# Kernel tuning notes

Measured on AMD Instinct MI355X. Metric: run time of the kernel, lower is better.

The kernel has to match this reference:

```python
import jax, jax.numpy as jnp
import numpy as np
from jax import lax

SIGMA = 0.8
THRESH_MIN = 50.0
THRESH_MAX = 80.0
TRACK_CONN = 5
TRACK_ITERS = 3


def _gaussian_kernel(sigma=SIGMA):
    ks = int(((sigma - 0.8) / 0.3 + 1) * 2 + 1)
    ks += 1 if ks % 2 == 0 else 0
    ax = np.arange(-ks // 2 + 1.0, ks // 2 + 1.0)
    xx, yy = np.meshgrid(ax, ax)
    normal = 1 / (2.0 * np.pi * sigma ** 2)
    k = np.exp(-(xx ** 2 + yy ** 2) / (2.0 * sigma ** 2)) * normal
    k = k / np.sum(k)
    return k.reshape(ks, ks, 1, 1).astype(np.float32)


def _sobel_kernel():
    gx = np.array([[-1, 0, 1], [-2, 0, 2], [-1, 0, 1]], dtype=np.float32)
    gy = np.array([[1, 2, 1], [0, 0, 0], [-1, -2, -1]], dtype=np.float32)
    return np.stack([gx, gy], axis=-1).reshape(3, 3, 1, 2)


def setup_inputs() -> dict:
    key = jax.random.key(0)
    x = jax.random.uniform(key, (8, 1024, 1024, 1), dtype=jnp.float32) * 255.0
    return {
        'x': x,
        'gaussian_kernel': jnp.asarray(_gaussian_kernel()),
        'sobel_kernel': jnp.asarray(_sobel_kernel()),
    }


def _conv_same(x, k):
    return lax.conv_general_dilated(x, k, (1, 1), 'SAME',
                                    dimension_numbers=('NHWC', 'HWIO', 'NHWC'))


# offsets with kernel value 0 (others are -inf) for the 4 angle NMS kernels
_ANGLE_OFFSETS = [
    [(0, -1), (0, 0), (0, 1)],     # 0 deg
    [(-1, 1), (0, 0), (1, -1)],    # 45 deg
    [(-1, 0), (0, 0), (1, 0)],     # 90 deg
    [(-1, -1), (0, 0), (1, 1)],    # 135 deg
]


def _angle_dilation(ar):
    # morphological dilation (tf.nn.dilation2d) with -inf masked 3x3 kernels,
    # realized as max over the 3 unmasked shifts per angle channel.
    B, H, W, _ = ar.shape
    pad = jnp.pad(ar, ((0, 0), (1, 1), (1, 1), (0, 0)),
                  constant_values=-jnp.inf)
    outs = []
    for c, offs in enumerate(_ANGLE_OFFSETS):
        ch = pad[..., c]
        m = ch[:, 1 + offs[0][0]:1 + offs[0][0] + H, 1 + offs[0][1]:1 + offs[0][1] + W]
        for dy, dx in offs[1:]:
            m = jnp.maximum(m, ch[:, 1 + dy:1 + dy + H, 1 + dx:1 + dx + W])
        outs.append(m)
    return jnp.stack(outs, axis=-1)


def _canny(x, gaussian_kernel, sobel_kernel):
    dt = x.dtype
    x_smooth = _conv_same(x, gaussian_kernel)
    grad_xy = _conv_same(x_smooth, sobel_kernel)
    gx, gy = grad_xy[..., 0:1], grad_xy[..., 1:2]
    theta = (jnp.arctan2(gy, gx) * (180.0 / np.pi) + 90.0) % 180.0
    grad_mag = jnp.clip(jnp.sqrt(gx * gx + gy * gy), 0.0, 255.0)

    # angle-bucketed masks (channels: 0, 45, 90, 135 deg)
    m0 = (theta >= 157.5) | (theta <= 22.5)
    m1 = (theta >= 22.5) & (theta < 67.5)
    m2 = (theta >= 67.5) & (theta < 112.5)
    m3 = (theta >= 112.5) & (theta < 157.5)
    masks = jnp.concatenate([m0, m1, m2, m3], axis=-1).astype(dt)
    angle_responses = masks * grad_mag  # (B,H,W,4)

    max_pool_angle = _angle_dilation(angle_responses)

    # non-max suppression + double threshold
    suppressed = jnp.where(max_pool_angle == angle_responses, grad_mag, 0.0)
    edge_candidates = jnp.max(suppressed, axis=-1, keepdims=True)
    strong = (edge_candidates >= THRESH_MAX).astype(dt)
    weak = ((edge_candidates >= THRESH_MIN) & (edge_candidates < THRESH_MAX)).astype(dt)

    # iterative hysteresis: weak pixels adjacent (within KxK window) to strong
    # pixels become strong
    win = (1, TRACK_CONN, TRACK_CONN, 1)
    for _ in range(TRACK_ITERS):
        pooled = lax.reduce_window(strong, -jnp.inf, lax.max, win,
                                   (1, 1, 1, 1), 'SAME')
        strong = jnp.clip(strong + weak * pooled, 0.0, 1.0)
    return strong.astype(dt)


def reference(x, gaussian_kernel, sobel_kernel):
    return _canny(x, gaussian_kernel, sobel_kernel)
```

## Files before the change

### kernel.cpp

```cpp
#include <hip/hip_runtime.h>
#include <math.h>

#define NT  512
#define TS  80
#define HX  9
#define XT2 98
#define ST2 96
#define MT2 94
#define WT2 92
#define HB  6
#define WPR 3

#define POOLA_BYTES ((MT2*MT2*4 + MT2*MT2 + 15) & ~15)

template<bool IN>
__device__ __forceinline__ void canny_tile(
    const float* __restrict__ xb, const float* __restrict__ g,
    float* __restrict__ ob, int H, int W, int ty0, int tx0, int tid,
    float* __restrict__ s_x, float* __restrict__ s_mag,
    unsigned char* __restrict__ s_dirb, float* __restrict__ s_sm,
    unsigned char* __restrict__ s_byte, unsigned int* __restrict__ s_bs,
    unsigned int* __restrict__ s_bw, unsigned int* __restrict__ s_bh)
{
  for (int i = tid; i < XT2*XT2; i += NT) {
    int r = i / XT2, c = i - r*XT2;
    int gy = ty0 + r - HX, gx = tx0 + c - HX;
    float v = 0.f;
    if (IN || ((unsigned)gy < (unsigned)H && (unsigned)gx < (unsigned)W))
      v = xb[(size_t)gy*W + gx];
    s_x[i] = v;
  }
  __syncthreads();

  for (int i = tid; i < ST2*(ST2/2); i += NT) {
    int r = i / (ST2/2), pc = i - r*(ST2/2);
    int c0 = 2*pc;
    const float* xr = &s_x[r*XT2 + c0];
    float2 q00 = *(const float2*)(xr),       q01 = *(const float2*)(xr+2);
    float2 q10 = *(const float2*)(xr+XT2),   q11 = *(const float2*)(xr+XT2+2);
    float2 q20 = *(const float2*)(xr+2*XT2), q21 = *(const float2*)(xr+2*XT2+2);
    int gy  = ty0 + r - (HX-1);
    int gx0 = tx0 + c0 - (HX-1);
    float a0 = 0.f, a1 = 0.f;
    if (IN || ((unsigned)gy < (unsigned)H && (unsigned)gx0 < (unsigned)W)) {
      float acc = 0.f;
      acc += q00.x*g[0]; acc += q00.y*g[1]; acc += q01.x*g[2];
      acc += q10.x*g[3]; acc += q10.y*g[4]; acc += q11.x*g[5];
      acc += q20.x*g[6]; acc += q20.y*g[7]; acc += q21.x*g[8];
      a0 = acc;
    }
    if (IN || ((unsigned)gy < (unsigned)H && (unsigned)(gx0+1) < (unsigned)W)) {
      float acc = 0.f;
      acc += q00.y*g[0]; acc += q01.x*g[1]; acc += q01.y*g[2];
      acc += q10.y*g[3]; acc += q11.x*g[4]; acc += q11.y*g[5];
      acc += q20.y*g[6]; acc += q21.x*g[7]; acc += q21.y*g[8];
      a1 = acc;
    }
    *(float2*)&s_sm[r*ST2 + c0] = make_float2(a0, a1);
  }
  __syncthreads();

  for (int i = tid; i < MT2*(MT2/2); i += NT) {
    int r = i / (MT2/2), pc = i - r*(MT2/2);
    int c0 = 2*pc;
    const float* sm0 = &s_sm[r*ST2 + c0];
    float2 p00=*(const float2*)(sm0),        p01=*(const float2*)(sm0+2);
    float2 p10=*(const float2*)(sm0+ST2),    p11=*(const float2*)(sm0+ST2+2);
    float2 p20=*(const float2*)(sm0+2*ST2),  p21=*(const float2*)(sm0+2*ST2+2);
    float v00=p00.x, v01=p00.y, v02=p01.x, v03=p01.y;
    float v10=p10.x, v11=p10.y, v12=p11.x, v13=p11.y;
    float v20=p20.x, v21=p20.y, v22=p21.x, v23=p21.y;
    unsigned int dpair = 0;
    float m0v = 0.f, m1v = 0.f;
    int gy  = ty0 + r - (HX-2);
    int gxb = tx0 + c0 - (HX-2);
#pragma unroll
    for (int half = 0; half < 2; ++half) {
      float a00 = half ? v01 : v00, a01 = half ? v02 : v01, a02 = half ? v03 : v02;
      float a10 = half ? v11 : v10,                          a12 = half ? v13 : v12;
      float a20 = half ? v21 : v20, a21 = half ? v22 : v21, a22 = half ? v23 : v22;
      float mag = 0.f; unsigned int dir = 0;
      if (IN || ((unsigned)gy < (unsigned)H && (unsigned)(gxb+half) < (unsigned)W)) {
        float fgx = 0.f - a00;
        fgx += a02;
        fgx = fmaf(a10, -2.f, fgx);
        fgx = fmaf(a12,  2.f, fgx);
        fgx -= a20;
        fgx += a22;
        float fgy = a00;
        fgy = fmaf(a01, 2.f, fgy);
        fgy += a02;
        fgy -= a20;
        fgy = fmaf(a21, -2.f, fgy);
        fgy -= a22;
        mag = fminf(sqrtf(fgx*fgx + fgy*fgy), 255.f);
        float ax = fabsf(fgx), ay = fabsf(fgy);
        float sum = ax + ay;
        float d1 = ay - 0.41421356237f*ax;
        float d2 = ay - 2.41421356237f*ax;
        float band = 1e-4f * sum;
        if (sum == 0.f) {
          dir = 4;
        } else if (fabsf(d1) >= band && fabsf(d2) >= band) {
          if (d2 > 0.f)      dir = 1;
          else if (d1 < 0.f) dir = 4;
          else dir = (((__float_as_uint(fgx) ^ __float_as_uint(fgy)) >> 31) & 1)
                       ? 2 : 8;
        } else {
          float th = atan2f(fgy, fgx) * 57.29577951308232f + 90.0f;
          if (th < 0.f) th += 180.f; else if (th >= 180.f) th -= 180.f;
          if (th >= 157.5f || th <= 22.5f)  dir |= 1;
          if (th >= 22.5f  && th < 67.5f)   dir |= 2;
          if (th >= 67.5f  && th < 112.5f)  dir |= 4;
          if (th >= 112.5f && th < 157.5f)  dir |= 8;
        }
      }
      if (half == 0) m0v = mag; else m1v = mag;
      dpair |= dir << (8*half);
    }
    *(float2*)&s_mag[r*MT2 + c0] = make_float2(m0v, m1v);
    *(unsigned short*)&s_dirb[r*MT2 + c0] = (unsigned short)dpair;
  }
  __syncthreads();

  for (int i = tid; i < WT2*(WT2/2); i += NT) {
    int r = i / (WT2/2), j = i - r*(WT2/2);
    int mr = r + 1;
    int cb = 2*j;
    const float* mrow = &s_mag[(mr-1)*MT2 + cb];
    float2 t0a = *(const float2*)(mrow),         t0b = *(const float2*)(mrow+2);
    float2 t1a = *(const float2*)(mrow+MT2),     t1b = *(const float2*)(mrow+MT2+2);
    float2 t2a = *(const float2*)(mrow+2*MT2),   t2b = *(const float2*)(mrow+2*MT2+2);
    const unsigned char* drow = &s_dirb[(mr-1)*MT2 + cb];
    unsigned int d0 = *(const unsigned short*)(drow)
                    | ((unsigned int)*(const unsigned short*)(drow+2) << 16);
    unsigned int d1 = *(const unsigned short*)(drow+MT2)
                    | ((unsigned int)*(const unsigned short*)(drow+MT2+2) << 16);
    unsigned int d2 = *(const unsigned short*)(drow+2*MT2)
                    | ((unsigned int)*(const unsigned short*)(drow+2*MT2+2) << 16);
    float m0[4] = {t0a.x, t0a.y, t0b.x, t0b.y};
    float m1[4] = {t1a.x, t1a.y, t1b.x, t1b.y};
    float m2[4] = {t2a.x, t2a.y, t2b.x, t2b.y};
    unsigned int out2 = 0;
#pragma unroll
    for (int k = 0; k < 2; ++k) {
      float mag = m1[k+1];
      unsigned int dc = (d1 >> (8*(k+1))) & 0xFu;
      bool keep = false;
      {
        float rp = (dc & 1) ? mag : 0.f;
        float a  = ((d1 >> (8*k))     & 1) ? m1[k]   : 0.f;
        float bb = ((d1 >> (8*(k+2))) & 1) ? m1[k+2] : 0.f;
        keep = keep || (a <= rp && bb <= rp);
      }
      {
        float rp = (dc & 2) ? mag : 0.f;
        float a  = ((d0 >> (8*(k+2))) & 2) ? m0[k+2] : 0.f;
        float bb = ((d2 >> (8*k))     & 2) ? m2[k]   : 0.f;
        keep = keep || (a <= rp && bb <= rp);
      }
      {
        float rp = (dc & 4) ? mag : 0.f;
        float a  = ((d0 >> (8*(k+1))) & 4) ? m0[k+1] : 0.f;
        float bb = ((d2 >> (8*(k+1))) & 4) ? m2[k+1] : 0.f;
        keep = keep || (a <= rp && bb <= rp);
      }
      {
        float rp = (dc & 8) ? mag : 0.f;
        float a  = ((d0 >> (8*k))     & 8) ? m0[k]   : 0.f;
        float bb = ((d2 >> (8*(k+2))) & 8) ? m2[k+2] : 0.f;
        keep = keep || (a <= rp && bb <= rp);
      }
      unsigned int v = keep ? ((mag >= 80.f) ? 2u : ((mag >= 50.f) ? 1u : 0u)) : 0u;
      out2 |= v << (8*k);
    }
    *(unsigned short*)&s_byte[r*WT2 + cb] = (unsigned short)out2;
  }
  __syncthreads();

  for (int i = tid; i < WT2*WPR; i += NT) {
    int r = i / WPR, k = i - r*WPR;
    unsigned int sb = 0, wb = 0;
    int cbase = k * 32;
#pragma unroll
    for (int jj = 0; jj < 32; ++jj) {
      int c = cbase + jj;
      unsigned int v = (c < WT2) ? s_byte[r*WT2 + c] : 0u;
      sb |= ((v >> 1) & 1u) << jj;
      wb |= (v & 1u) << jj;
    }
    s_bs[r*WPR + k] = sb;
    s_bw[r*WPR + k] = wb;
  }
  __syncthreads();

#pragma unroll
  for (int it = 0; it < 3; ++it) {
    for (int i = tid; i < WT2*WPR; i += NT) {
      int r = i / WPR, k = i - r*WPR;
      unsigned int s  = s_bs[r*WPR + k];
      unsigned int lo = (k > 0)     ? s_bs[r*WPR + k - 1] : 0u;
      unsigned int hi = (k < WPR-1) ? s_bs[r*WPR + k + 1] : 0u;
      s_bh[r*WPR + k] = s | (s<<1) | (s<<2) | (s>>1) | (s>>2)
                          | (lo>>30) | (lo>>31) | (hi<<30) | (hi<<31);
    }
    __syncthreads();
    for (int i = tid; i < (WT2-4)*WPR; i += NT) {
      int r = i / WPR + 2, k = i - (r-2)*WPR;
      unsigned int p = s_bh[(r-2)*WPR + k] | s_bh[(r-1)*WPR + k] | s_bh[r*WPR + k]
                     | s_bh[(r+1)*WPR + k] | s_bh[(r+2)*WPR + k];
      s_bs[r*WPR + k] |= (s_bw[r*WPR + k] & p);
    }
    __syncthreads();
  }

  for (int i = tid; i < TS*TS; i += NT) {
    int r = i / TS, c = i - r*TS;
    int oy = ty0 + r, ox = tx0 + c;
    if (IN || (oy < H && ox < W)) {
      int rr = r + HB, cc = c + HB;
      unsigned int w = s_bs[rr*WPR + (cc >> 5)];
      ob[(size_t)oy*W + ox] = (float)((w >> (cc & 31)) & 1u);
    }
  }
}

__global__ __launch_bounds__(NT) void canny_fused(
    const float* __restrict__ x, const float* __restrict__ gk,
    float* __restrict__ out, int H, int W, int tilesX, int tilesY)
{
  __shared__ __align__(16) unsigned char poolA[POOLA_BYTES];
  float* s_x   = (float*)poolA;
  float* s_mag = (float*)poolA;
  unsigned char* s_dirb = poolA + MT2*MT2*4;
  __shared__ __align__(16) float s_sm[ST2*ST2];
  unsigned char* s_byte = (unsigned char*)s_sm;
  unsigned int* s_bs = (unsigned int*)((unsigned char*)s_sm + 8464);
  unsigned int* s_bw = s_bs + WT2*WPR;
  unsigned int* s_bh = s_bw + WT2*WPR;

  const int tpi = tilesX * tilesY;
  const int b  = blockIdx.x / tpi;
  const int t  = blockIdx.x % tpi;
  const int ty0 = (t / tilesX) * TS;
  const int tx0 = (t % tilesX) * TS;
  const float* xb = x + (size_t)b * H * W;
  float* ob = out + (size_t)b * H * W;
  const int tid = threadIdx.x;

  float g[9];
#pragma unroll
  for (int i = 0; i < 9; ++i) g[i] = gk[i];

  const bool interior = (ty0 >= HX) && (ty0 + XT2 - HX <= H)
                     && (tx0 >= HX) && (tx0 + XT2 - HX <= W);
  if (interior)
    canny_tile<true >(xb, g, ob, H, W, ty0, tx0, tid,
                      s_x, s_mag, s_dirb, s_sm, s_byte, s_bs, s_bw, s_bh);
  else
    canny_tile<false>(xb, g, ob, H, W, ty0, tx0, tid,
                      s_x, s_mag, s_dirb, s_sm, s_byte, s_bs, s_bw, s_bh);
}

extern "C" void kernel_launch(void* const* d_in, const int* in_sizes, int n_in,
                              void* d_out, int out_size, void* d_ws, size_t ws_size,
                              hipStream_t stream)
{
  const float* x  = (const float*)d_in[0];
  const float* gk = (const float*)d_in[1];
  float* out = (float*)d_out;

  const int H = 1024, W = 1024;
  const int B = in_sizes[0] / (H * W);
  const int tilesX = (W + TS - 1) / TS, tilesY = (H + TS - 1) / TS;

  dim3 grid(B * tilesX * tilesY);
  canny_fused<<<grid, NT, 0, stream>>>(x, gk, out, H, W, tilesX, tilesY);
}
```

Before: 151.8 us.

## Shrink tiles to 64, pack directions as nibbles, vectorize bit packing and stores

Reduces the output tile from 80 to 64 so it aligns with the 1024 image, which removes ragged edge tiles and allows float4 stores of the final mask on interior tiles. Direction codes are packed two per byte to cut shared memory, the byte-to-bitmask packing uses a multiply trick on 32-bit words instead of per-byte loops, and shared arrays get padded strides. Smaller tiles increase the halo overhead relative to the useful output, and the smaller shared footprint may allow more blocks resident per CU.

```diff
diff --git a/kernel.cpp b/kernel.cpp
--- a/kernel.cpp
+++ b/kernel.cpp
@@ -1,29 +1,32 @@
 #include <hip/hip_runtime.h>
 #include <math.h>
 
-#define NT  512
-#define TS  80
-#define HX  9
-#define XT2 98
-#define ST2 96
-#define MT2 94
-#define WT2 92
-#define HB  6
-#define WPR 3
-
-#define POOLA_BYTES ((MT2*MT2*4 + MT2*MT2 + 15) & ~15)
+#define NT   512
+#define TS   64
+#define HX   9
+#define XR   82
+#define XSTR 84
+#define ST   80
+#define SSTR 82
+#define MT   78
+#define DSTR 39
+#define WT   76
+#define WPR  3
+#define HB   6
+
+#define POOLA ((XR*XSTR*4 + 15) & ~15)
 
 template<bool IN>
 __device__ __forceinline__ void canny_tile(
     const float* __restrict__ xb, const float* __restrict__ g,
     float* __restrict__ ob, int H, int W, int ty0, int tx0, int tid,
     float* __restrict__ s_x, float* __restrict__ s_mag,
-    unsigned char* __restrict__ s_dirb, float* __restrict__ s_sm,
+    unsigned char* __restrict__ s_dirn, float* __restrict__ s_sm,
     unsigned char* __restrict__ s_byte, unsigned int* __restrict__ s_bs,
     unsigned int* __restrict__ s_bw, unsigned int* __restrict__ s_bh)
 {
-  for (int i = tid; i < XT2*XT2; i += NT) {
-    int r = i / XT2, c = i - r*XT2;
+  for (int i = tid; i < XR*XSTR; i += NT) {
+    int r = i / XSTR, c = i - r*XSTR;
     int gy = ty0 + r - HX, gx = tx0 + c - HX;
     float v = 0.f;
     if (IN || ((unsigned)gy < (unsigned)H && (unsigned)gx < (unsigned)W))
@@ -32,13 +35,13 @@
   }
   __syncthreads();
 
-  for (int i = tid; i < ST2*(ST2/2); i += NT) {
-    int r = i / (ST2/2), pc = i - r*(ST2/2);
+  for (int i = tid; i < ST*(ST/2); i += NT) {
+    int r = i / (ST/2), pc = i - r*(ST/2);
     int c0 = 2*pc;
-    const float* xr = &s_x[r*XT2 + c0];
-    float2 q00 = *(const float2*)(xr),       q01 = *(const float2*)(xr+2);
-    float2 q10 = *(const float2*)(xr+XT2),   q11 = *(const float2*)(xr+XT2+2);
-    float2 q20 = *(const float2*)(xr+2*XT2), q21 = *(const float2*)(xr+2*XT2+2);
+    const float* xr = &s_x[r*XSTR + c0];
+    float2 q00 = *(const float2*)(xr),        q01 = *(const float2*)(xr+2);
+    float2 q10 = *(const float2*)(xr+XSTR),   q11 = *(const float2*)(xr+XSTR+2);
+    float2 q20 = *(const float2*)(xr+2*XSTR), q21 = *(const float2*)(xr+2*XSTR+2);
     int gy  = ty0 + r - (HX-1);
     int gx0 = tx0 + c0 - (HX-1);
     float a0 = 0.f, a1 = 0.f;
@@ -56,17 +59,17 @@
       acc += q20.y*g[6]; acc += q21.x*g[7]; acc += q21.y*g[8];
       a1 = acc;
     }
-    *(float2*)&s_sm[r*ST2 + c0] = make_float2(a0, a1);
-  }
-  __syncthreads();
-
-  for (int i = tid; i < MT2*(MT2/2); i += NT) {
-    int r = i / (MT2/2), pc = i - r*(MT2/2);
+    *(float2*)&s_sm[r*SSTR + c0] = make_float2(a0, a1);
+  }
+  __syncthreads();
+
+  for (int i = tid; i < MT*(MT/2); i += NT) {
+    int r = i / (MT/2), pc = i - r*(MT/2);
     int c0 = 2*pc;
-    const float* sm0 = &s_sm[r*ST2 + c0];
-    float2 p00=*(const float2*)(sm0),        p01=*(const float2*)(sm0+2);
-    float2 p10=*(const float2*)(sm0+ST2),    p11=*(const float2*)(sm0+ST2+2);
-    float2 p20=*(const float2*)(sm0+2*ST2),  p21=*(const float2*)(sm0+2*ST2+2);
+    const float* sm0 = &s_sm[r*SSTR + c0];
+    float2 p00=*(const float2*)(sm0),         p01=*(const float2*)(sm0+2);
+    float2 p10=*(const float2*)(sm0+SSTR),    p11=*(const float2*)(sm0+SSTR+2);
+    float2 p20=*(const float2*)(sm0+2*SSTR),  p21=*(const float2*)(sm0+2*SSTR+2);
     float v00=p00.x, v01=p00.y, v02=p01.x, v03=p01.y;
     float v10=p10.x, v11=p10.y, v12=p11.x, v13=p11.y;
     float v20=p20.x, v21=p20.y, v22=p21.x, v23=p21.y;
@@ -116,28 +119,24 @@
         }
       }
       if (half == 0) m0v = mag; else m1v = mag;
-      dpair |= dir << (8*half);
-    }
-    *(float2*)&s_mag[r*MT2 + c0] = make_float2(m0v, m1v);
-    *(unsigned short*)&s_dirb[r*MT2 + c0] = (unsigned short)dpair;
-  }
-  __syncthreads();
-
-  for (int i = tid; i < WT2*(WT2/2); i += NT) {
-    int r = i / (WT2/2), j = i - r*(WT2/2);
-    int mr = r + 1;
+      dpair |= dir << (4*half);
+    }
+    *(float2*)&s_mag[r*MT + c0] = make_float2(m0v, m1v);
+    s_dirn[r*DSTR + pc] = (unsigned char)dpair;
+  }
+  __syncthreads();
+
+  for (int i = tid; i < WT*(WT/2); i += NT) {
+    int r = i / (WT/2), j = i - r*(WT/2);
     int cb = 2*j;
-    const float* mrow = &s_mag[(mr-1)*MT2 + cb];
-    float2 t0a = *(const float2*)(mrow),         t0b = *(const float2*)(mrow+2);
-    float2 t1a = *(const float2*)(mrow+MT2),     t1b = *(const float2*)(mrow+MT2+2);
-    float2 t2a = *(const float2*)(mrow+2*MT2),   t2b = *(const float2*)(mrow+2*MT2+2);
-    const unsigned char* drow = &s_dirb[(mr-1)*MT2 + cb];
-    unsigned int d0 = *(const unsigned short*)(drow)
-                    | ((unsigned int)*(const unsigned short*)(drow+2) << 16);
-    unsigned int d1 = *(const unsigned short*)(drow+MT2)
-                    | ((unsigned int)*(const unsigned short*)(drow+MT2+2) << 16);
-    unsigned int d2 = *(const unsigned short*)(drow+2*MT2)
-                    | ((unsigned int)*(const unsigned short*)(drow+2*MT2+2) << 16);
+    const float* mrow = &s_mag[r*MT + cb];
+    float2 t0a = *(const float2*)(mrow),        t0b = *(const float2*)(mrow+2);
+    float2 t1a = *(const float2*)(mrow+MT),     t1b = *(const float2*)(mrow+MT+2);
+    float2 t2a = *(const float2*)(mrow+2*MT),   t2b = *(const float2*)(mrow+2*MT+2);
+    const unsigned char* drow = &s_dirn[r*DSTR + j];
+    unsigned int d0 = drow[0]        | ((unsigned int)drow[1] << 8);
+    unsigned int d1 = drow[DSTR]     | ((unsigned int)drow[DSTR+1] << 8);
+    unsigned int d2 = drow[2*DSTR]   | ((unsigned int)drow[2*DSTR+1] << 8);
     float m0[4] = {t0a.x, t0a.y, t0b.x, t0b.y};
     float m1[4] = {t1a.x, t1a.y, t1b.x, t1b.y};
     float m2[4] = {t2a.x, t2a.y, t2b.x, t2b.y};
@@ -145,49 +144,53 @@
 #pragma unroll
     for (int k = 0; k < 2; ++k) {
       float mag = m1[k+1];
-      unsigned int dc = (d1 >> (8*(k+1))) & 0xFu;
+      unsigned int dc = (d1 >> (4*(k+1))) & 0xFu;
       bool keep = false;
       {
         float rp = (dc & 1) ? mag : 0.f;
-        float a  = ((d1 >> (8*k))     & 1) ? m1[k]   : 0.f;
-        float bb = ((d1 >> (8*(k+2))) & 1) ? m1[k+2] : 0.f;
+        float a  = ((d1 >> (4*k))     & 1) ? m1[k]   : 0.f;
+        float bb = ((d1 >> (4*(k+2))) & 1) ? m1[k+2] : 0.f;
         keep = keep || (a <= rp && bb <= rp);
       }
       {
         float rp = (dc & 2) ? mag : 0.f;
-        float a  = ((d0 >> (8*(k+2))) & 2) ? m0[k+2] : 0.f;
-        float bb = ((d2 >> (8*k))     & 2) ? m2[k]   : 0.f;
+        float a  = ((d0 >> (4*(k+2))) & 2) ? m0[k+2] : 0.f;
+        float bb = ((d2 >> (4*k))     & 2) ? m2[k]   : 0.f;
         keep = keep || (a <= rp && bb <= rp);
       }
       {
         float rp = (dc & 4) ? mag : 0.f;
-        float a  = ((d0 >> (8*(k+1))) & 4) ? m0[k+1] : 0.f;
-        float bb = ((d2 >> (8*(k+1))) & 4) ? m2[k+1] : 0.f;
+        float a  = ((d0 >> (4*(k+1))) & 4) ? m0[k+1] : 0.f;
+        float bb = ((d2 >> (4*(k+1))) & 4) ? m2[k+1] : 0.f;
         keep = keep || (a <= rp && bb <= rp);
       }
       {
         float rp = (dc & 8) ? mag : 0.f;
-        float a  = ((d0 >> (8*k))     & 8) ? m0[k]   : 0.f;
-        float bb = ((d2 >> (8*(k+2))) & 8) ? m2[k+2] : 0.f;
+        float a  = ((d0 >> (4*k))     & 8) ? m0[k]   : 0.f;
+        float bb = ((d2 >> (4*(k+2))) & 8) ? m2[k+2] : 0.f;
         keep = keep || (a <= rp && bb <= rp);
       }
       unsigned int v = keep ? ((mag >= 80.f) ? 2u : ((mag >= 50.f) ? 1u : 0u)) : 0u;
       out2 |= v << (8*k);
     }
-    *(unsigned short*)&s_byte[r*WT2 + cb] = (unsigned short)out2;
-  }
-  __syncthreads();
-
-  for (int i = tid; i < WT2*WPR; i += NT) {
+    *(unsigned short*)&s_byte[r*WT + cb] = (unsigned short)out2;
+  }
+  __syncthreads();
+
+  for (int i = tid; i < WT*WPR; i += NT) {
     int r = i / WPR, k = i - r*WPR;
+    const unsigned char* row = &s_byte[r*WT + 32*k];
+    int nw = (k < 2) ? 8 : 3;
     unsigned int sb = 0, wb = 0;
-    int cbase = k * 32;
-#pragma unroll
-    for (int jj = 0; jj < 32; ++jj) {
-      int c = cbase + jj;
-      unsigned int v = (c < WT2) ? s_byte[r*WT2 + c] : 0u;
-      sb |= ((v >> 1) & 1u) << jj;
-      wb |= (v & 1u) << jj;
+#pragma unroll
+    for (int q = 0; q < 8; ++q) {
+      if (q < nw) {
+        unsigned int w = *(const unsigned int*)(row + 4*q);
+        unsigned int t = (w >> 1) & 0x01010101u;
+        unsigned int u = w & 0x01010101u;
+        sb |= (((t * 0x01020408u) >> 24) & 0xFu) << (4*q);
+        wb |= (((u * 0x01020408u) >> 24) & 0xFu) << (4*q);
+      }
     }
     s_bs[r*WPR + k] = sb;
     s_bw[r*WPR + k] = wb;
@@ -196,7 +199,7 @@
 
 #pragma unroll
   for (int it = 0; it < 3; ++it) {
-    for (int i = tid; i < WT2*WPR; i += NT) {
+    for (int i = tid; i < WT*WPR; i += NT) {
       int r = i / WPR, k = i - r*WPR;
       unsigned int s  = s_bs[r*WPR + k];
       unsigned int lo = (k > 0)     ? s_bs[r*WPR + k - 1] : 0u;
@@ -205,7 +208,7 @@
                           | (lo>>30) | (lo>>31) | (hi<<30) | (hi<<31);
     }
     __syncthreads();
-    for (int i = tid; i < (WT2-4)*WPR; i += NT) {
+    for (int i = tid; i < (WT-4)*WPR; i += NT) {
       int r = i / WPR + 2, k = i - (r-2)*WPR;
       unsigned int p = s_bh[(r-2)*WPR + k] | s_bh[(r-1)*WPR + k] | s_bh[r*WPR + k]
                      | s_bh[(r+1)*WPR + k] | s_bh[(r+2)*WPR + k];
@@ -214,13 +217,31 @@
     __syncthreads();
   }
 
-  for (int i = tid; i < TS*TS; i += NT) {
-    int r = i / TS, c = i - r*TS;
-    int oy = ty0 + r, ox = tx0 + c;
-    if (IN || (oy < H && ox < W)) {
-      int rr = r + HB, cc = c + HB;
-      unsigned int w = s_bs[rr*WPR + (cc >> 5)];
-      ob[(size_t)oy*W + ox] = (float)((w >> (cc & 31)) & 1u);
+  if (IN) {
+    for (int i = tid; i < TS*(TS/4); i += NT) {
+      int r = i >> 4, mq = i & 15;
+      int cc0 = 4*mq + HB;
+      int rr = r + HB;
+      int k0 = cc0 >> 5;
+      unsigned long long wp = (unsigned long long)s_bs[rr*WPR + k0]
+                            | ((unsigned long long)s_bs[rr*WPR + k0 + 1] << 32);
+      unsigned int bits = (unsigned int)(wp >> (cc0 & 31));
+      float4 o;
+      o.x = (float)(bits & 1u);
+      o.y = (float)((bits >> 1) & 1u);
+      o.z = (float)((bits >> 2) & 1u);
+      o.w = (float)((bits >> 3) & 1u);
+      *(float4*)&ob[(size_t)(ty0+r)*W + tx0 + 4*mq] = o;
+    }
+  } else {
+    for (int i = tid; i < TS*TS; i += NT) {
+      int r = i / TS, c = i - r*TS;
+      int oy = ty0 + r, ox = tx0 + c;
+      if (oy < H && ox < W) {
+        int rr = r + HB, cc = c + HB;
+        unsigned int w = s_bs[rr*WPR + (cc >> 5)];
+        ob[(size_t)oy*W + ox] = (float)((w >> (cc & 31)) & 1u);
+      }
     }
   }
 }
@@ -229,15 +250,15 @@
     const float* __restrict__ x, const float* __restrict__ gk,
     float* __restrict__ out, int H, int W, int tilesX, int tilesY)
 {
-  __shared__ __align__(16) unsigned char poolA[POOLA_BYTES];
+  __shared__ __align__(16) unsigned char poolA[POOLA];
   float* s_x   = (float*)poolA;
   float* s_mag = (float*)poolA;
-  unsigned char* s_dirb = poolA + MT2*MT2*4;
-  __shared__ __align__(16) float s_sm[ST2*ST2];
+  unsigned char* s_dirn = poolA + MT*MT*4;
+  __shared__ __align__(16) float s_sm[ST*SSTR];
   unsigned char* s_byte = (unsigned char*)s_sm;
-  unsigned int* s_bs = (unsigned int*)((unsigned char*)s_sm + 8464);
-  unsigned int* s_bw = s_bs + WT2*WPR;
-  unsigned int* s_bh = s_bw + WT2*WPR;
+  unsigned int* s_bs = (unsigned int*)((unsigned char*)s_sm + 5776);
+  unsigned int* s_bw = s_bs + WT*WPR;
+  unsigned int* s_bh = s_bw + WT*WPR;
 
   const int tpi = tilesX * tilesY;
   const int b  = blockIdx.x / tpi;
@@ -252,14 +273,14 @@
 #pragma unroll
   for (int i = 0; i < 9; ++i) g[i] = gk[i];
 
-  const bool interior = (ty0 >= HX) && (ty0 + XT2 - HX <= H)
-                     && (tx0 >= HX) && (tx0 + XT2 - HX <= W);
+  const bool interior = (ty0 >= HX) && (ty0 + XR - HX <= H)
+                     && (tx0 >= HX) && (tx0 + XSTR - HX < W);
   if (interior)
     canny_tile<true >(xb, g, ob, H, W, ty0, tx0, tid,
-                      s_x, s_mag, s_dirb, s_sm, s_byte, s_bs, s_bw, s_bh);
+                      s_x, s_mag, s_dirn, s_sm, s_byte, s_bs, s_bw, s_bh);
   else
     canny_tile<false>(xb, g, ob, H, W, ty0, tx0, tid,
-                      s_x, s_mag, s_dirb, s_sm, s_byte, s_bs, s_bw, s_bh);
+                      s_x, s_mag, s_dirn, s_sm, s_byte, s_bs, s_bw, s_bh);
 }
 
 extern "C" void kernel_launch(void* const* d_in, const int* in_sizes, int n_in,
```

After: 146.6 us. -3.4%, faster.
